# Kernel tuning notes

Measured on AMD Instinct MI355X. Metric: run time of the kernel, lower is better.

Reference implementation:

```python
import jax, jax.numpy as jnp
import numpy as np

EPS = 1e-5

def conv1x1(x, W, b):
    # x: (B,C,H,W), W: (O,C), b: (O,)
    return jnp.einsum('bchw,oc->bohw', x, W) + b[None, :, None, None]

def setup_inputs() -> dict:
    key = jax.random.key(0)
    ks = jax.random.split(key, 16)
    B, C_in, C1, D, K, H, Wd = 8, 512, 256, 128, 32, 96, 96
    s = lambda k, shape, fan: jax.random.normal(k, shape, jnp.float32) * (1.0 / np.sqrt(fan))
    return {
        'X': jax.random.normal(ks[0], (B, C_in, H, Wd), jnp.float32),
        'W_theta': s(ks[1], (C1, C_in), C_in), 'b_theta': jnp.zeros((C1,), jnp.float32),
        'W_phi': s(ks[2], (C1, C_in), C_in), 'b_phi': jnp.zeros((C1,), jnp.float32),
        'W_g': s(ks[3], (C1, C_in), C_in), 'b_g': jnp.zeros((C1,), jnp.float32),
        'W2': s(ks[4], (C_in, C1), C1), 'b2': jnp.zeros((C_in,), jnp.float32),
        'W3': s(ks[5], (D, C_in), C_in), 'b3': jnp.zeros((D,), jnp.float32),
        'codewords': jax.random.normal(ks[6], (K, D), jnp.float32),
        'scale': -jax.random.uniform(ks[7], (K,), jnp.float32),  # Deep-TEN init: U(-1,0)
        'W_fc': s(ks[8], (C_in, D), D), 'b_fc': jnp.zeros((C_in,), jnp.float32),
    }

def reference(X, W_theta, b_theta, W_phi, b_phi, W_g, b_g, W2, b2, W3, b3,
              codewords, scale, W_fc, b_fc):
    B, C_in, H, Wd = X.shape
    C1 = W_theta.shape[0]
    D, K = W3.shape[0], codewords.shape[0]
    N = H * Wd
    # --- non-local (channel-attention) block ---
    theta = conv1x1(X, W_theta, b_theta).reshape(B, C1, N)          # (B,C1,N)
    phi = conv1x1(X, W_phi, b_phi).reshape(B, C1, N)                # (B,C1,N)
    g = conv1x1(X, W_g, b_g).reshape(B, C1, N)                      # (B,C1,N)
    f = jax.nn.softmax(jnp.einsum('bcn,bdn->bcd', theta, phi), axis=-1)  # (B,C1,C1)
    y = jnp.einsum('bcd,bdn->bcn', f, g).reshape(B, C1, H, Wd)
    z = conv1x1(y, W2, b2) + X                                      # (B,C_in,H,W)
    # --- Deep-TEN encoding ---
    z_ = conv1x1(z, W3, b3)                                         # (B,D,H,W)
    x = z_.reshape(B, D, N).transpose(0, 2, 1)                      # (B,N,D)
    # squared L2 distances to codewords without (B,N,K,D) residuals
    dist = (jnp.sum(x * x, -1, keepdims=True)
            - 2.0 * jnp.einsum('bnd,kd->bnk', x, codewords)
            + jnp.sum(codewords * codewords, -1))                   # (B,N,K)
    A = jax.nn.softmax(scale * dist, axis=-1)                       # (B,N,K)
    # E_k = sum_i A_ik (x_i - c_k)
    E = jnp.einsum('bnk,bnd->bkd', A, x) - A.sum(1)[..., None] * codewords  # (B,K,D)
    # --- training-mode batch norm over K channels (no affine) ---
    mean = E.mean(axis=(0, 2), keepdims=True)
    var = E.var(axis=(0, 2), keepdims=True)
    e = jax.nn.relu((E - mean) * jax.lax.rsqrt(var + EPS))
    Es = e.sum(axis=1)                                              # (B,D)
    gamma = jax.nn.sigmoid(Es @ W_fc.T + b_fc)                      # (B,C_in)
    return z * gamma[:, :, None, None]
```

## Files before the change

kernel.cpp:

```cpp
#include <hip/hip_runtime.h>


typedef unsigned short u16;

#define Bb 8
#define Cc 512
#define C1 256
#define Dd 128
#define Kk 32
#define Nn 9216

typedef __attribute__((ext_vector_type(8))) short short8v;
typedef __attribute__((ext_vector_type(4))) short short4v;
typedef __attribute__((ext_vector_type(4))) float f32x4;

__device__ __forceinline__ float b2f(u16 u) {
  union { unsigned int i; float f; } v; v.i = ((unsigned int)u) << 16; return v.f;
}
__device__ __forceinline__ u16 f2b(float f) {
  union { float f; unsigned int i; } v; v.f = f;
  unsigned int x = v.i;
  return (u16)((x + 0x7fffu + ((x >> 16) & 1u)) >> 16);
}

__device__ __forceinline__ float4 load4(const float* p) { return *(const float4*)p; }
__device__ __forceinline__ float4 load4(const u16* p) {
  ushort4 q = *(const ushort4*)p;
  return make_float4(b2f(q.x), b2f(q.y), b2f(q.z), b2f(q.w));
}
__device__ __forceinline__ void store4(float* p, float a, float b, float c, float d) {
  *(float4*)p = make_float4(a, b, c, d);
}

__device__ __forceinline__ float waveSum(float v) {
  #pragma unroll
  for (int o = 32; o > 0; o >>= 1) v += __shfl_xor(v, o);
  return v;
}
__device__ __forceinline__ float waveMax(float v) {
  #pragma unroll
  for (int o = 32; o > 0; o >>= 1) v = fmaxf(v, __shfl_xor(v, o));
  return v;
}
__device__ __forceinline__ float blockSum256(float v) {
  __shared__ float sm[4];
  v = waveSum(v);
  if ((threadIdx.x & 63) == 0) sm[threadIdx.x >> 6] = v;
  __syncthreads();
  float r = sm[0] + sm[1] + sm[2] + sm[3];
  __syncthreads();
  return r;
}
__device__ __forceinline__ float blockMax256(float v) {
  __shared__ float sm[4];
  v = waveMax(v);
  if ((threadIdx.x & 63) == 0) sm[threadIdx.x >> 6] = v;
  __syncthreads();
  float r = fmaxf(fmaxf(sm[0], sm[1]), fmaxf(sm[2], sm[3]));
  __syncthreads();
  return r;
}

__device__ __forceinline__ f32x4 mfma_bf16_16x16x32(short8v a, short8v b, f32x4 c) {
  asm("v_mfma_f32_16x16x32_bf16 %0, %1, %2, %0" : "+v"(c) : "v"(a), "v"(b));
  return c;
}

__device__ __forceinline__ int fsw(int r) { return (r ^ (r >> 2) ^ (r >> 4)) & 3; }

__device__ __forceinline__ void cvt2(float x0, float x1, unsigned int& h, unsigned int& l) {
  asm("v_cvt_pk_bf16_f32 %0, %1, %2" : "=v"(h) : "v"(x0), "v"(x1));
  union { unsigned int u; float f; } fa, fb;
  fa.u = h << 16; fb.u = h & 0xffff0000u;
  float r0 = x0 - fa.f, r1 = x1 - fb.f;
  asm("v_cvt_pk_bf16_f32 %0, %1, %2" : "=v"(l) : "v"(r0), "v"(r1));
}

__device__ __forceinline__ void storeC4(float* p, float4 v) { *(float4*)p = v; }
__device__ __forceinline__ void storeC4(u16* p, float4 v) {
  ushort4 q; q.x = f2b(v.x); q.y = f2b(v.y); q.z = f2b(v.z); q.w = f2b(v.w);
  *(ushort4*)p = q;
}

template<typename TO, int NF, int OMODE>
__global__ __launch_bounds__(256, 2) void gemm_mfma(
    const float* __restrict__ A, const float* __restrict__ B, TO* __restrict__ C,
    int N, int K,
    long long sA, long long sB, long long sC,
    const float* __restrict__ biasRow, long long sBias,
    const float* __restrict__ scaleRow,
    int gnx, int gny)
{
  static_assert(NF == 8, "NF");
  constexpr int BN = 32 * NF;
  __shared__ __align__(16) u16 Asm_[2][128][40];
  __shared__ __align__(16) u16 Bsm_[2][BN][40];

  int id = blockIdx.x;
  {
    const int nwg = gridDim.x;
    if ((nwg & 7) == 0) id = (id & 7) * (nwg >> 3) + (id >> 3);
  }
  const int per = gnx * gny;
  const int b = id / per;
  const int rem = id - b * per;
  const int by = rem % gny;
  const int bx = rem / gny;
  A += b * sA; B += b * sB; C += b * sC;
  const int m0 = by * 128, n0 = bx * BN;

  const int t = threadIdx.x;
  const int w = t >> 6, lane = t & 63;
  const int wr = w >> 1, wc = w & 1;
  const int lr = lane & 15, lq = lane >> 4;

  const int sar = t >> 1, sak = (t & 1) * 16;
  const int kg = t >> 5, ng = t & 31;

  float ra[16];
  float rb[32];

  auto loadA = [&](int k0) {
    const float* p = A + (long long)(m0 + sar) * K + (k0 + sak);
    #pragma unroll
    for (int i = 0; i < 4; ++i) {
      float4 v = *(const float4*)(p + i * 4);
      ra[i*4+0] = v.x; ra[i*4+1] = v.y; ra[i*4+2] = v.z; ra[i*4+3] = v.w;
    }
  };
  auto loadB = [&](int k0) {
    const float* p = B + (long long)(k0 + kg * 4) * N + (n0 + ng * 8);
    #pragma unroll
    for (int i = 0; i < 4; ++i) {
      float4 v0 = *(const float4*)(p + (long long)i * N);
      float4 v1 = *(const float4*)(p + (long long)i * N + 4);
      rb[i*8+0]=v0.x; rb[i*8+1]=v0.y; rb[i*8+2]=v0.z; rb[i*8+3]=v0.w;
      rb[i*8+4]=v1.x; rb[i*8+5]=v1.y; rb[i*8+6]=v1.z; rb[i*8+7]=v1.w;
    }
  };

  auto stage = [&]() {
    {
      const int f = fsw(sar);
      #pragma unroll
      for (int h = 0; h < 2; ++h) {
        const int col = ((((sak >> 3) + h) ^ f) << 3);
        union { unsigned int u[4]; short8v v; } H, L;
        #pragma unroll
        for (int p = 0; p < 4; ++p) cvt2(ra[h*8+2*p], ra[h*8+2*p+1], H.u[p], L.u[p]);
        *(short8v*)&Asm_[0][sar][col] = H.v;
        *(short8v*)&Asm_[1][sar][col] = L.v;
      }
    }
    {
      #pragma unroll
      for (int j = 0; j < 8; ++j) {
        const int n = ng * 8 + j;
        const int col = (((kg >> 1) ^ fsw(n)) << 3) + (kg & 1) * 4;
        union { unsigned int u[2]; short4v v; } H, L;
        #pragma unroll
        for (int p = 0; p < 2; ++p)
          cvt2(rb[(2*p)*8 + j], rb[(2*p+1)*8 + j], H.u[p], L.u[p]);
        *(short4v*)&Bsm_[0][n][col] = H.v;
        *(short4v*)&Bsm_[1][n][col] = L.v;
      }
    }
  };

  f32x4 acc[4][NF];
  #pragma unroll
  for (int im = 0; im < 4; ++im)
    #pragma unroll
    for (int in = 0; in < NF; ++in)
      acc[im][in] = f32x4{0.f, 0.f, 0.f, 0.f};

  loadA(0); loadB(0);
  for (int k0 = 0; k0 < K; k0 += 32) {
    stage();
    if (k0 + 32 < K) { loadA(k0 + 32); loadB(k0 + 32); }
    __syncthreads();
    short8v af[2][4];
    #pragma unroll
    for (int im = 0; im < 4; ++im) {
      const int r = wr * 64 + im * 16 + lr;
      const int col = ((lq ^ fsw(r)) << 3);
      af[0][im] = *(const short8v*)&Asm_[0][r][col];
      af[1][im] = *(const short8v*)&Asm_[1][r][col];
    }
    #pragma unroll
    for (int in = 0; in < NF; ++in) {
      const int rB = wc * NF * 16 + in * 16 + lr;
      const int colB = ((lq ^ fsw(rB)) << 3);
      short8v bh = *(const short8v*)&Bsm_[0][rB][colB];
      short8v bl = *(const short8v*)&Bsm_[1][rB][colB];
      #pragma unroll
      for (int im = 0; im < 4; ++im) {
        acc[im][in] = mfma_bf16_16x16x32(af[0][im], bh, acc[im][in]);
        acc[im][in] = mfma_bf16_16x16x32(af[0][im], bl, acc[im][in]);
        acc[im][in] = mfma_bf16_16x16x32(af[1][im], bh, acc[im][in]);
      }
    }
    __syncthreads();
  }
  asm volatile("s_nop 7\n\ts_nop 7\n\ts_nop 7");

  if constexpr (OMODE == 1) {
    const float* bb = biasRow + (long long)b * sBias;
    #pragma unroll
    for (int im = 0; im < 4; ++im) {
      #pragma unroll
      for (int in = 0; in < NF; ++in) {
        const f32x4 a = acc[im][in];
        const int gc = n0 + wc * NF * 16 + in * 16 + lr;
        const int d0b = wr * 64 + im * 16 + lq * 4;
        float4 v = make_float4(a[0] + bb[d0b + 0], a[1] + bb[d0b + 1],
                               a[2] + bb[d0b + 2], a[3] + bb[d0b + 3]);
        storeC4(&C[(long long)gc * Dd + d0b], v);
      }
    }
  } else {
    #pragma unroll
    for (int im = 0; im < 4; ++im) {
      #pragma unroll
      for (int in = 0; in < NF; ++in) {
        const f32x4 a = acc[im][in];
        const int gc = n0 + wc * NF * 16 + in * 16 + lr;
        #pragma unroll
        for (int p = 0; p < 4; ++p) {
          const int gr = m0 + wr * 64 + im * 16 + lq * 4 + p;
          float v = a[p];
          if (biasRow) v += biasRow[b * sBias + gr];
          if (scaleRow) v *= scaleRow[b * sBias + gr];
          C[(long long)gr * N + gc] = v;
        }
      }
    }
  }
}

__device__ __constant__ int PIa[10] = {0,0,0,0,1,1,1,2,2,3};
__device__ __constant__ int PJa[10] = {0,1,2,3,1,2,3,2,3,3};

__global__ __launch_bounds__(256, 2) void gxxt_kernel(
    const float* __restrict__ X, float* __restrict__ part,
    int numKS, int kChunk)
{
  __shared__ __align__(16) u16 Asm_[2][128][40];
  __shared__ __align__(16) u16 Bsm_[2][128][40];

  int id = blockIdx.x;
  {
    const int nwg = gridDim.x;
    if ((nwg & 7) == 0) id = (id & 7) * (nwg >> 3) + (id >> 3);
  }
  const int pair = id % 10;
  const int rest = id / 10;
  const int ks = rest % numKS;
  const int b = rest / numKS;
  const int i0 = PIa[pair] * 128, j0 = PJa[pair] * 128;
  const bool same = (i0 == j0);
  const float* Xb = X + (long long)b * Cc * Nn;
  const int kBeg = ks * kChunk, kEnd = kBeg + kChunk;

  const int t = threadIdx.x;
  const int w = t >> 6, lane = t & 63;
  const int wr = w >> 1, wc = w & 1;
  const int lr = lane & 15, lq = lane >> 4;
  const int sar = t >> 1, sak = (t & 1) * 16;

  float ra[16], rb[16];

  auto loadA = [&](int k0) {
    const float* p = Xb + (long long)(i0 + sar) * Nn + (k0 + sak);
    #pragma unroll
    for (int i = 0; i < 4; ++i) {
      float4 v = *(const float4*)(p + i * 4);
      ra[i*4+0] = v.x; ra[i*4+1] = v.y; ra[i*4+2] = v.z; ra[i*4+3] = v.w;
    }
  };
  auto loadB = [&](int k0) {
    const float* p = Xb + (long long)(j0 + sar) * Nn + (k0 + sak);
    #pragma unroll
    for (int i = 0; i < 4; ++i) {
      float4 v = *(const float4*)(p + i * 4);
      rb[i*4+0] = v.x; rb[i*4+1] = v.y; rb[i*4+2] = v.z; rb[i*4+3] = v.w;
    }
  };
  auto stageRow = [&](const float* s16, u16 (*H)[40], u16 (*L)[40]) {
    const int f = fsw(sar);
    #pragma unroll
    for (int h = 0; h < 2; ++h) {
      const int col = ((((sak >> 3) + h) ^ f) << 3);
      union { unsigned int u[4]; short8v v; } Hv, Lv;
      #pragma unroll
      for (int p = 0; p < 4; ++p) cvt2(s16[h*8+2*p], s16[h*8+2*p+1], Hv.u[p], Lv.u[p]);
      *(short8v*)&H[sar][col] = Hv.v;
      *(short8v*)&L[sar][col] = Lv.v;
    }
  };

  const u16 (*BH)[40] = same ? Asm_[0] : Bsm_[0];
  const u16 (*BL)[40] = same ? Asm_[1] : Bsm_[1];

  f32x4 acc[4][4];
  #pragma unroll
  for (int im = 0; im < 4; ++im)
    #pragma unroll
    for (int in = 0; in < 4; ++in)
      acc[im][in] = f32x4{0.f, 0.f, 0.f, 0.f};

  loadA(kBeg);
  if (!same) loadB(kBeg);
  for (int k0 = kBeg; k0 < kEnd; k0 += 32) {
    stageRow(ra, Asm_[0], Asm_[1]);
    if (!same) stageRow(rb, Bsm_[0], Bsm_[1]);
    if (k0 + 32 < kEnd) { loadA(k0 + 32); if (!same) loadB(k0 + 32); }
    __syncthreads();
    short8v af[2][4];
    #pragma unroll
    for (int im = 0; im < 4; ++im) {
      const int r = wr * 64 + im * 16 + lr;
      const int col = ((lq ^ fsw(r)) << 3);
      af[0][im] = *(const short8v*)&Asm_[0][r][col];
      af[1][im] = *(const short8v*)&Asm_[1][r][col];
    }
    #pragma unroll
    for (int in = 0; in < 4; ++in) {
      const int rB = wc * 64 + in * 16 + lr;
      const int colB = ((lq ^ fsw(rB)) << 3);
      short8v bh = *(const short8v*)&BH[rB][colB];
      short8v bl = *(const short8v*)&BL[rB][colB];
      #pragma unroll
      for (int im = 0; im < 4; ++im) {
        acc[im][in] = mfma_bf16_16x16x32(af[0][im], bh, acc[im][in]);
        acc[im][in] = mfma_bf16_16x16x32(af[0][im], bl, acc[im][in]);
        acc[im][in] = mfma_bf16_16x16x32(af[1][im], bh, acc[im][in]);
      }
    }
    __syncthreads();
  }
  asm volatile("s_nop 7\n\ts_nop 7\n\ts_nop 7");

  float* Cp = part + ((long long)(ks * Bb + b) * 10 + pair) * 16384;
  #pragma unroll
  for (int im = 0; im < 4; ++im) {
    #pragma unroll
    for (int in = 0; in < 4; ++in) {
      const f32x4 a = acc[im][in];
      const int gc = wc * 64 + in * 16 + lr;
      #pragma unroll
      for (int p = 0; p < 4; ++p) {
        const int gr = wr * 64 + im * 16 + lq * 4 + p;
        Cp[gr * 128 + gc] = a[p];
      }
    }
  }
}

__global__ __launch_bounds__(256) void gred_kernel(const float* __restrict__ part,
    float* __restrict__ G, int numKS) {
  __shared__ float sm[64][129];
  const int pair = blockIdx.x % 10, b = blockIdx.x / 10;
  const int i0 = PIa[pair] * 128, j0 = PJa[pair] * 128;
  float* Gb = G + (long long)b * Cc * Cc;
  const long long ksStr = (long long)Bb * 10 * 16384;
  const float* p0 = part + ((long long)b * 10 + pair) * 16384;
  const int t = threadIdx.x;
  for (int half = 0; half < 2; ++half) {
    const int r0 = half * 64;
    __syncthreads();
    for (int rep = 0; rep < 32; ++rep) {
      int idx = r0 * 128 + rep * 256 + t;
      float s = 0.f;
      for (int ks = 0; ks < numKS; ++ks) s += p0[(long long)ks * ksStr + idx];
      int r = (idx >> 7) - r0, c = idx & 127;
      sm[r][c] = s;
      Gb[(long long)(i0 + r0 + r) * Cc + (j0 + c)] = s;
    }
    if (i0 != j0) {
      __syncthreads();
      for (int rep = 0; rep < 32; ++rep) {
        int o = rep * 256 + t;
        int rr = o >> 6, cc = o & 63;
        Gb[(long long)(j0 + rr) * Cc + (i0 + r0 + cc)] = sm[cc][rr];
      }
    }
  }
}

template<bool TRANSB>
__global__ __launch_bounds__(256) void gemm64(
    const float* __restrict__ A, const float* __restrict__ B, float* __restrict__ C,
    int M, int N, int K,
    long long sA, long long sB, long long sC,
    const float* __restrict__ biasRow, long long sBias)
{
  const int bz = blockIdx.z;
  A += (long long)bz * sA;
  B += (long long)bz * sB;
  C += (long long)bz * sC;
  const int m0 = blockIdx.y * 64, n0 = blockIdx.x * 64;
  __shared__ __align__(16) float As[16][64];
  __shared__ __align__(16) float Bs[16][64];
  const int t = threadIdx.x;
  const int lr = t >> 2, lk = (t & 3) << 2;
  const int tm = (t >> 4) << 2, tn = (t & 15) << 2;
  float acc[4][4] = {};
  for (int k0 = 0; k0 < K; k0 += 16) {
    {
      float4 a = load4(A + (long long)(m0 + lr) * K + (k0 + lk));
      As[lk + 0][lr] = a.x; As[lk + 1][lr] = a.y; As[lk + 2][lr] = a.z; As[lk + 3][lr] = a.w;
    }
    if (TRANSB) {
      float4 b = load4(B + (long long)(n0 + lr) * K + (k0 + lk));
      Bs[lk + 0][lr] = b.x; Bs[lk + 1][lr] = b.y; Bs[lk + 2][lr] = b.z; Bs[lk + 3][lr] = b.w;
    } else {
      const int kr = t >> 4, nc = (t & 15) << 2;
      float4 b = load4(B + (long long)(k0 + kr) * N + (n0 + nc));
      *(float4*)&Bs[kr][nc] = b;
    }
    __syncthreads();
    #pragma unroll
    for (int kk = 0; kk < 16; ++kk) {
      const float4 av = *(const float4*)&As[kk][tm];
      const float4 bv = *(const float4*)&Bs[kk][tn];
      acc[0][0] = fmaf(av.x, bv.x, acc[0][0]);
      acc[0][1] = fmaf(av.x, bv.y, acc[0][1]);
      acc[0][2] = fmaf(av.x, bv.z, acc[0][2]);
      acc[0][3] = fmaf(av.x, bv.w, acc[0][3]);
      acc[1][0] = fmaf(av.y, bv.x, acc[1][0]);
      acc[1][1] = fmaf(av.y, bv.y, acc[1][1]);
      acc[1][2] = fmaf(av.y, bv.z, acc[1][2]);
      acc[1][3] = fmaf(av.y, bv.w, acc[1][3]);
      acc[2][0] = fmaf(av.z, bv.x, acc[2][0]);
      acc[2][1] = fmaf(av.z, bv.y, acc[2][1]);
      acc[2][2] = fmaf(av.z, bv.z, acc[2][2]);
      acc[2][3] = fmaf(av.z, bv.w, acc[2][3]);
      acc[3][0] = fmaf(av.w, bv.x, acc[3][0]);
      acc[3][1] = fmaf(av.w, bv.y, acc[3][1]);
      acc[3][2] = fmaf(av.w, bv.z, acc[3][2]);
      acc[3][3] = fmaf(av.w, bv.w, acc[3][3]);
    }
    __syncthreads();
  }
  #pragma unroll
  for (int i = 0; i < 4; ++i) {
    const int m = m0 + tm + i;
    float bias = biasRow ? biasRow[bz * sBias + m] : 0.f;
    store4(C + (long long)m * N + (n0 + tn),
           acc[i][0] + bias, acc[i][1] + bias, acc[i][2] + bias, acc[i][3] + bias);
  }
}

__global__ __launch_bounds__(256) void rowsum_kernel(const float* __restrict__ X,
                                                     float* __restrict__ s, int N) {
  long long row = blockIdx.x;
  const float* p = X + row * N;
  float acc = 0.f;
  for (int i = threadIdx.x; i < N; i += 256) acc += p[i];
  acc = blockSum256(acc);
  if (threadIdx.x == 0) s[row] = acc;
}

__global__ __launch_bounds__(256) void gemv512_kernel(const float* __restrict__ W,
                                                      const float* __restrict__ s,
                                                      float* __restrict__ out) {
  int b = blockIdx.x;
  __shared__ float ssm[Cc];
  for (int i = threadIdx.x; i < Cc; i += 256) ssm[i] = s[b * Cc + i];
  __syncthreads();
  int i = threadIdx.x;
  const float* wr = W + i * Cc;
  float acc = 0.f;
  for (int k = 0; k < Cc; ++k) acc = fmaf(wr[k], ssm[k], acc);
  out[b * C1 + i] = acc;
}

__global__ __launch_bounds__(256) void softmax_kernel(float* __restrict__ L,
    const float* __restrict__ bth, const float* __restrict__ bph,
    const float* __restrict__ u, const float* __restrict__ v) {
  int row = blockIdx.x;
  int b = row >> 8, i = row & 255;
  int j = threadIdx.x;
  float bt = bth[i], bp = bph[j];
  long long idx = (long long)row * C1 + j;
  float val = L[idx] + bt * v[b * C1 + j] + u[b * C1 + i] * bp + (float)Nn * bt * bp;
  float mx = blockMax256(val);
  float p = expf(val - mx);
  float sm = blockSum256(p);
  L[idx] = p / sm;
}

__global__ __launch_bounds__(256) void w_kernel(const float* __restrict__ f,
                                                const float* __restrict__ bg,
                                                float* __restrict__ w) {
  int b = blockIdx.x;
  __shared__ float bgs[C1];
  bgs[threadIdx.x] = bg[threadIdx.x];
  __syncthreads();
  int i = threadIdx.x;
  const float* fr = f + ((long long)b * C1 + i) * C1;
  float acc = 0.f;
  for (int j = 0; j < C1; ++j) acc = fmaf(fr[j], bgs[j], acc);
  w[b * C1 + i] = acc;
}

__global__ __launch_bounds__(256) void q_kernel(const float* __restrict__ W2,
                                                const float* __restrict__ b2v,
                                                const float* __restrict__ w,
                                                float* __restrict__ q) {
  int gi = blockIdx.x * 256 + threadIdx.x;
  int b = gi >> 9, c = gi & 511;
  __shared__ float wsm[C1];
  wsm[threadIdx.x] = w[b * C1 + threadIdx.x];
  __syncthreads();
  const float* wr = W2 + c * C1;
  float acc = b2v[c];
  for (int i = 0; i < C1; ++i) acc = fmaf(wr[i], wsm[i], acc);
  q[gi] = acc;
}

__global__ __launch_bounds__(256) void adddiag_kernel(float* __restrict__ P) {
  int gi = blockIdx.x * 256 + threadIdx.x;
  int b = gi >> 9, c = gi & 511;
  P[((long long)b * Cc + c) * Cc + c] += 1.f;
}

__global__ __launch_bounds__(256) void zqbias_kernel(const float* __restrict__ W3,
    const float* __restrict__ b3, const float* __restrict__ q, float* __restrict__ zqb) {
  int gi = blockIdx.x * 256 + threadIdx.x;
  int b = gi >> 7, d = gi & 127;
  const float* wr = W3 + d * Cc;
  const float* qr = q + b * Cc;
  float acc = b3[d];
  for (int c = 0; c < Cc; ++c) acc = fmaf(wr[c], qr[c], acc);
  zqb[gi] = acc;
}

template<typename ZT>
__global__ __launch_bounds__(256) void enc_kernel(
    const ZT* __restrict__ zq,
    const float* __restrict__ cw,
    const float* __restrict__ sc,
    float* __restrict__ Eraw,
    float* __restrict__ Asum)
{
  __shared__ float csm[Kk][Dd + 1];
  __shared__ float cc[Kk], ssm[Kk];
  __shared__ float sA[Kk][256 + 1];
  __shared__ float zs[16][Dd + 4];
  const int tid = threadIdx.x;
  const int b = blockIdx.y;
  const int n0 = blockIdx.x * 256;

  #pragma unroll
  for (int r = 0; r < 16; ++r) {
    int idx = r * 256 + tid;
    csm[idx >> 7][idx & 127] = cw[idx];
  }
  if (tid < Kk) ssm[tid] = sc[tid];
  __syncthreads();
  if (tid < Kk) {
    float a = 0.f;
    for (int d = 0; d < Dd; ++d) { float cv = csm[tid][d]; a = fmaf(cv, cv, a); }
    cc[tid] = a;
  }
  __syncthreads();

  const ZT* zrow = zq + ((long long)b * Nn + n0 + tid) * Dd;
  float dots[Kk];
  #pragma unroll
  for (int k = 0; k < Kk; ++k) dots[k] = 0.f;
  float xx = 0.f;
  for (int d = 0; d < Dd; d += 4) {
    float4 xv = load4(zrow + d);
    xx = fmaf(xv.x, xv.x, xx); xx = fmaf(xv.y, xv.y, xx);
    xx = fmaf(xv.z, xv.z, xx); xx = fmaf(xv.w, xv.w, xx);
    #pragma unroll
    for (int k = 0; k < Kk; ++k) {
      float dk = dots[k];
      dk = fmaf(csm[k][d + 0], xv.x, dk);
      dk = fmaf(csm[k][d + 1], xv.y, dk);
      dk = fmaf(csm[k][d + 2], xv.z, dk);
      dk = fmaf(csm[k][d + 3], xv.w, dk);
      dots[k] = dk;
    }
  }
  float mx = -1e30f;
  #pragma unroll
  for (int k = 0; k < Kk; ++k) {
    float l = ssm[k] * (xx - 2.f * dots[k] + cc[k]);
    dots[k] = l;
    mx = fmaxf(mx, l);
  }
  float sum = 0.f;
  #pragma unroll
  for (int k = 0; k < Kk; ++k) { float p = expf(dots[k] - mx); dots[k] = p; sum += p; }
  float inv = 1.f / sum;
  #pragma unroll
  for (int k = 0; k < Kk; ++k) sA[k][tid] = dots[k] * inv;
  __syncthreads();
  if (tid < Kk) {
    float s = 0.f;
    for (int p = 0; p < 256; ++p) s += sA[tid][p];
    atomicAdd(&Asum[b * Kk + tid], s);
  }

  float acc[16];
  #pragma unroll
  for (int j = 0; j < 16; ++j) acc[j] = 0.f;
  const int k = tid & 31, d0 = (tid >> 5) * 16;
  const int spx = tid >> 4, sd = (tid & 15) * 8;
  for (int it = 0; it < 16; ++it) {
    __syncthreads();
    {
      const ZT* src = zq + ((long long)b * Nn + n0 + it * 16 + spx) * Dd + sd;
      float4 a4 = load4(src);
      float4 b4 = load4(src + 4);
      *(float4*)&zs[spx][sd] = a4;
      *(float4*)&zs[spx][sd + 4] = b4;
    }
    __syncthreads();
    #pragma unroll
    for (int p = 0; p < 16; ++p) {
      float a = sA[k][it * 16 + p];
      #pragma unroll
      for (int j = 0; j < 16; ++j) acc[j] = fmaf(a, zs[p][d0 + j], acc[j]);
    }
  }
  float* Ep = Eraw + ((long long)b * Kk + k) * Dd + d0;
  #pragma unroll
  for (int j = 0; j < 16; ++j) atomicAdd(Ep + j, acc[j]);
}

__global__ __launch_bounds__(256) void bn_kernel(const float* __restrict__ Eraw,
    const float* __restrict__ Asum, const float* __restrict__ cw, float* __restrict__ Es) {
  int k = blockIdx.x, tid = threadIdx.x;
  float vals[4], s = 0.f, s2 = 0.f;
  #pragma unroll
  for (int r = 0; r < 4; ++r) {
    int i = r * 256 + tid;
    int b = i >> 7, d = i & 127;
    float e = Eraw[((long long)b * Kk + k) * Dd + d] - Asum[b * Kk + k] * cw[k * Dd + d];
    vals[r] = e; s += e; s2 = fmaf(e, e, s2);
  }
  s = blockSum256(s);
  s2 = blockSum256(s2);
  float mean = s * (1.f / 1024.f);
  float var = fmaxf(s2 * (1.f / 1024.f) - mean * mean, 0.f);
  float rs = rsqrtf(var + 1e-5f);
  #pragma unroll
  for (int r = 0; r < 4; ++r) {
    int i = r * 256 + tid;
    int b = i >> 7, d = i & 127;
    float e = (vals[r] - mean) * rs;
    if (e > 0.f) atomicAdd(&Es[b * Dd + d], e);
  }
}

__global__ __launch_bounds__(256) void gamma_kernel(const float* __restrict__ Es,
    const float* __restrict__ Wfc, const float* __restrict__ bfc, float* __restrict__ gam) {
  int gi = blockIdx.x * 256 + threadIdx.x;
  int b = gi >> 9, c = gi & 511;
  __shared__ float esm[Dd];
  if (threadIdx.x < Dd) esm[threadIdx.x] = Es[b * Dd + threadIdx.x];
  __syncthreads();
  const float* wr = Wfc + c * Dd;
  float acc = bfc[c];
  for (int d = 0; d < Dd; ++d) acc = fmaf(wr[d], esm[d], acc);
  gam[gi] = 1.f / (1.f + expf(-acc));
}

extern "C" void kernel_launch(void* const* d_in, const int* in_sizes, int n_in,
                              void* d_out, int out_size, void* d_ws, size_t ws_size,
                              hipStream_t stream) {
  const float* X   = (const float*)d_in[0];
  const float* Wth = (const float*)d_in[1];
  const float* bth = (const float*)d_in[2];
  const float* Wph = (const float*)d_in[3];
  const float* bph = (const float*)d_in[4];
  const float* Wg  = (const float*)d_in[5];
  const float* bg  = (const float*)d_in[6];
  const float* W2  = (const float*)d_in[7];
  const float* b2v = (const float*)d_in[8];
  const float* W3  = (const float*)d_in[9];
  const float* b3v = (const float*)d_in[10];
  const float* CW  = (const float*)d_in[11];
  const float* SC  = (const float*)d_in[12];
  const float* Wfc = (const float*)d_in[13];
  const float* bfc = (const float*)d_in[14];
  float* out = (float*)d_out;
  float* wsf = (float*)d_ws;

  const long long szL   = (long long)Bb * C1 * C1;
  const long long szRA  = (long long)Bb * Cc * Cc;
  const long long szRB  = (long long)Bb * C1 * Cc;
  long long off = 0;
  float* s_   = wsf + off; off += Bb * Cc;
  float* u_   = wsf + off; off += Bb * C1;
  float* v_   = wsf + off; off += Bb * C1;
  float* w_   = wsf + off; off += Bb * C1;
  float* q_   = wsf + off; off += Bb * Cc;
  float* Eraw_= wsf + off; off += (long long)Bb * Kk * Dd;
  float* Es_  = wsf + off; off += Bb * Dd;
  float* Asum_= wsf + off; off += Bb * Kk;
  float* gam_ = wsf + off; off += Bb * Cc;
  float* L_   = wsf + off; off += szL;
  float* regA = wsf + off; off += szRA;
  float* regB = wsf + off; off += szRB;
  const long long baseFloats = off;
  float* tail = wsf + off;
  const long long ZQ_F  = (long long)Bb * Dd * Nn;
  const long long tailFloats = (long long)(ws_size / 4) - baseFloats;
  const bool big = tailFloats >= ZQ_F;
  const int numKS = big ? 6 : 2;
  float* part = tail;
  float* zqf  = tail;
  u16*   zqh  = (u16*)tail;
  float* R_   = L_;
  float* zqb_ = u_;

  const long long strX = (long long)Cc * Nn;
  const long long sG = (long long)Cc * Cc;
  const long long sU = (long long)C1 * Cc;
  const long long sL = (long long)C1 * C1;
  const long long sR = (long long)Dd * Cc;

  rowsum_kernel<<<Bb * Cc, 256, 0, stream>>>(X, s_, Nn);
  gxxt_kernel<<<dim3(10 * numKS * Bb), 256, 0, stream>>>(X, part, numKS, Nn / numKS);
  gred_kernel<<<dim3(10 * Bb), 256, 0, stream>>>(part, regA, numKS);
  gemm_mfma<float, 8, 0><<<dim3(32), 256, 0, stream>>>(
      Wth, regA, regB, Cc, Cc, 0, sG, sU, nullptr, 0, nullptr, 2, 2);
  gemv512_kernel<<<Bb, 256, 0, stream>>>(Wth, s_, u_);
  gemv512_kernel<<<Bb, 256, 0, stream>>>(Wph, s_, v_);
  gemm64<true><<<dim3(4, 4, Bb), 256, 0, stream>>>(
      regB, Wph, L_, C1, C1, Cc, sU, 0, sL, nullptr, 0);
  softmax_kernel<<<Bb * C1, 256, 0, stream>>>(L_, bth, bph, u_, v_);
  w_kernel<<<Bb, 256, 0, stream>>>(L_, bg, w_);
  gemm_mfma<float, 8, 0><<<dim3(32), 256, 0, stream>>>(
      L_, Wg, regB, Cc, C1, sL, 0, sU, nullptr, 0, nullptr, 2, 2);
  q_kernel<<<16, 256, 0, stream>>>(W2, b2v, w_, q_);
  gemm_mfma<float, 8, 0><<<dim3(64), 256, 0, stream>>>(
      W2, regB, regA, Cc, C1, 0, sU, sG, nullptr, 0, nullptr, 2, 4);
  adddiag_kernel<<<16, 256, 0, stream>>>(regA);
  gemm_mfma<float, 8, 0><<<dim3(16), 256, 0, stream>>>(
      W3, regA, R_, Cc, Cc, 0, sG, sR, nullptr, 0, nullptr, 2, 1);
  zqbias_kernel<<<4, 256, 0, stream>>>(W3, b3v, q_, zqb_);
  hipMemsetAsync(Eraw_, 0, (size_t)(Bb * Kk * Dd + Bb * Dd + Bb * Kk) * 4, stream);
  if (big) {
    gemm_mfma<float, 8, 1><<<dim3(288), 256, 0, stream>>>(
        R_, X, zqf, Nn, Cc, sR, strX, (long long)Dd * Nn, zqb_, Dd, nullptr, 36, 1);
    enc_kernel<float><<<dim3(36, Bb), 256, 0, stream>>>(zqf, CW, SC, Eraw_, Asum_);
  } else {
    gemm_mfma<u16, 8, 1><<<dim3(288), 256, 0, stream>>>(
        R_, X, zqh, Nn, Cc, sR, strX, (long long)Dd * Nn, zqb_, Dd, nullptr, 36, 1);
    enc_kernel<u16><<<dim3(36, Bb), 256, 0, stream>>>(zqh, CW, SC, Eraw_, Asum_);
  }
  bn_kernel<<<Kk, 256, 0, stream>>>(Eraw_, Asum_, CW, Es_);
  gamma_kernel<<<16, 256, 0, stream>>>(Es_, Wfc, bfc, gam_);
  gemm_mfma<float, 8, 0><<<dim3(1152), 256, 0, stream>>>(
      regA, X, out, Nn, Cc, sG, strX, strX, q_, Cc, gam_, 36, 4);
  (void)in_sizes; (void)n_in; (void)out_size;
}
```

Before: 1.096 ms.

## Fuse small kernels, fold gamma into P, and spread encoding atomics over slots

Merges the two gemv launches into one and folds the w reduction into the softmax kernel. The +I diagonal moves into the W2 GEMM epilogue, and gamma is pre-applied to P and q so the final GEMM epilogue no longer scales each element. The encoding accumulators are split into 8 slot copies that bn_kernel reduces, which cuts atomic contention in enc_kernel. This trades a few launches and the per-element scale load for an extra pass over P (scaleP) and a larger zeroing memset.

```diff
diff --git a/kernel.cpp b/kernel.cpp
--- a/kernel.cpp
+++ b/kernel.cpp
@@ -82,13 +82,12 @@
   *(ushort4*)p = q;
 }
 
-template<typename TO, int NF, int OMODE>
+template<typename TO, int NF, int OMODE, bool ADDI>
 __global__ __launch_bounds__(256, 2) void gemm_mfma(
     const float* __restrict__ A, const float* __restrict__ B, TO* __restrict__ C,
     int N, int K,
     long long sA, long long sB, long long sC,
     const float* __restrict__ biasRow, long long sBias,
-    const float* __restrict__ scaleRow,
     int gnx, int gny)
 {
   static_assert(NF == 8, "NF");
@@ -230,7 +229,7 @@
           const int gr = m0 + wr * 64 + im * 16 + lq * 4 + p;
           float v = a[p];
           if (biasRow) v += biasRow[b * sBias + gr];
-          if (scaleRow) v *= scaleRow[b * sBias + gr];
+          if (ADDI && gr == gc) v += 1.f;
           C[(long long)gr * N + gc] = v;
         }
       }
@@ -462,10 +461,12 @@
   if (threadIdx.x == 0) s[row] = acc;
 }
 
-__global__ __launch_bounds__(256) void gemv512_kernel(const float* __restrict__ W,
-                                                      const float* __restrict__ s,
-                                                      float* __restrict__ out) {
-  int b = blockIdx.x;
+__global__ __launch_bounds__(256) void gemv2_kernel(const float* __restrict__ Wth,
+    const float* __restrict__ Wph, const float* __restrict__ s,
+    float* __restrict__ u, float* __restrict__ v) {
+  int b = blockIdx.x & 7, sel = blockIdx.x >> 3;
+  const float* W = sel ? Wph : Wth;
+  float* out = sel ? v : u;
   __shared__ float ssm[Cc];
   for (int i = threadIdx.x; i < Cc; i += 256) ssm[i] = s[b * Cc + i];
   __syncthreads();
@@ -478,31 +479,23 @@
 
 __global__ __launch_bounds__(256) void softmax_kernel(float* __restrict__ L,
     const float* __restrict__ bth, const float* __restrict__ bph,
-    const float* __restrict__ u, const float* __restrict__ v) {
+    const float* __restrict__ u, const float* __restrict__ v,
+    const float* __restrict__ bg, float* __restrict__ w) {
+  __shared__ float bgs[C1];
   int row = blockIdx.x;
   int b = row >> 8, i = row & 255;
   int j = threadIdx.x;
+  bgs[j] = bg[j];
   float bt = bth[i], bp = bph[j];
   long long idx = (long long)row * C1 + j;
   float val = L[idx] + bt * v[b * C1 + j] + u[b * C1 + i] * bp + (float)Nn * bt * bp;
   float mx = blockMax256(val);
   float p = expf(val - mx);
   float sm = blockSum256(p);
-  L[idx] = p / sm;
-}
-
-__global__ __launch_bounds__(256) void w_kernel(const float* __restrict__ f,
-                                                const float* __restrict__ bg,
-                                                float* __restrict__ w) {
-  int b = blockIdx.x;
-  __shared__ float bgs[C1];
-  bgs[threadIdx.x] = bg[threadIdx.x];
-  __syncthreads();
-  int i = threadIdx.x;
-  const float* fr = f + ((long long)b * C1 + i) * C1;
-  float acc = 0.f;
-  for (int j = 0; j < C1; ++j) acc = fmaf(fr[j], bgs[j], acc);
-  w[b * C1 + i] = acc;
+  float f = p / sm;
+  L[idx] = f;
+  float ws = blockSum256(f * bgs[j]);
+  if (j == 0) w[row] = ws;
 }
 
 __global__ __launch_bounds__(256) void q_kernel(const float* __restrict__ W2,
@@ -518,12 +511,6 @@
   float acc = b2v[c];
   for (int i = 0; i < C1; ++i) acc = fmaf(wr[i], wsm[i], acc);
   q[gi] = acc;
-}
-
-__global__ __launch_bounds__(256) void adddiag_kernel(float* __restrict__ P) {
-  int gi = blockIdx.x * 256 + threadIdx.x;
-  int b = gi >> 9, c = gi & 511;
-  P[((long long)b * Cc + c) * Cc + c] += 1.f;
 }
 
 __global__ __launch_bounds__(256) void zqbias_kernel(const float* __restrict__ W3,
@@ -542,8 +529,8 @@
     const ZT* __restrict__ zq,
     const float* __restrict__ cw,
     const float* __restrict__ sc,
-    float* __restrict__ Eraw,
-    float* __restrict__ Asum)
+    float* __restrict__ Eraw8,
+    float* __restrict__ Asum8)
 {
   __shared__ float csm[Kk][Dd + 1];
   __shared__ float cc[Kk], ssm[Kk];
@@ -551,6 +538,7 @@
   __shared__ float zs[16][Dd + 4];
   const int tid = threadIdx.x;
   const int b = blockIdx.y;
+  const int slot = blockIdx.x & 7;
   const int n0 = blockIdx.x * 256;
 
   #pragma unroll
@@ -603,7 +591,7 @@
   if (tid < Kk) {
     float s = 0.f;
     for (int p = 0; p < 256; ++p) s += sA[tid][p];
-    atomicAdd(&Asum[b * Kk + tid], s);
+    atomicAdd(&Asum8[((long long)slot * Bb + b) * Kk + tid], s);
   }
 
   float acc[16];
@@ -628,20 +616,30 @@
       for (int j = 0; j < 16; ++j) acc[j] = fmaf(a, zs[p][d0 + j], acc[j]);
     }
   }
-  float* Ep = Eraw + ((long long)b * Kk + k) * Dd + d0;
+  float* Ep = Eraw8 + (((long long)slot * Bb + b) * Kk + k) * Dd + d0;
   #pragma unroll
   for (int j = 0; j < 16; ++j) atomicAdd(Ep + j, acc[j]);
 }
 
-__global__ __launch_bounds__(256) void bn_kernel(const float* __restrict__ Eraw,
-    const float* __restrict__ Asum, const float* __restrict__ cw, float* __restrict__ Es) {
+__global__ __launch_bounds__(256) void bn_kernel(const float* __restrict__ Eraw8,
+    const float* __restrict__ Asum8, const float* __restrict__ cw, float* __restrict__ Es) {
+  __shared__ float sas[8];
   int k = blockIdx.x, tid = threadIdx.x;
+  if (tid < 8) {
+    float a = 0.f;
+    for (int sl = 0; sl < 8; ++sl) a += Asum8[((long long)sl * Bb + tid) * Kk + k];
+    sas[tid] = a;
+  }
+  __syncthreads();
   float vals[4], s = 0.f, s2 = 0.f;
   #pragma unroll
   for (int r = 0; r < 4; ++r) {
     int i = r * 256 + tid;
     int b = i >> 7, d = i & 127;
-    float e = Eraw[((long long)b * Kk + k) * Dd + d] - Asum[b * Kk + k] * cw[k * Dd + d];
+    float e = 0.f;
+    for (int sl = 0; sl < 8; ++sl)
+      e += Eraw8[(((long long)sl * Bb + b) * Kk + k) * Dd + d];
+    e -= sas[b] * cw[k * Dd + d];
     vals[r] = e; s += e; s2 = fmaf(e, e, s2);
   }
   s = blockSum256(s);
@@ -659,7 +657,8 @@
 }
 
 __global__ __launch_bounds__(256) void gamma_kernel(const float* __restrict__ Es,
-    const float* __restrict__ Wfc, const float* __restrict__ bfc, float* __restrict__ gam) {
+    const float* __restrict__ Wfc, const float* __restrict__ bfc,
+    float* __restrict__ gam, float* __restrict__ q) {
   int gi = blockIdx.x * 256 + threadIdx.x;
   int b = gi >> 9, c = gi & 511;
   __shared__ float esm[Dd];
@@ -668,7 +667,18 @@
   const float* wr = Wfc + c * Dd;
   float acc = bfc[c];
   for (int d = 0; d < Dd; ++d) acc = fmaf(wr[d], esm[d], acc);
-  gam[gi] = 1.f / (1.f + expf(-acc));
+  float g = 1.f / (1.f + expf(-acc));
+  gam[gi] = g;
+  q[gi] *= g;
+}
+
+__global__ __launch_bounds__(256) void scaleP_kernel(float* __restrict__ P,
+    const float* __restrict__ gam) {
+  long long f = ((long long)blockIdx.x * 256 + threadIdx.x) * 4;
+  int b = (int)(f >> 18), c = (int)((f >> 9) & 511);
+  float g = gam[b * Cc + c];
+  float4 v = *(const float4*)(P + f);
+  store4(P + f, v.x * g, v.y * g, v.z * g, v.w * g);
 }
 
 extern "C" void kernel_launch(void* const* d_in, const int* in_sizes, int n_in,
@@ -719,6 +729,9 @@
   u16*   zqh  = (u16*)tail;
   float* R_   = L_;
   float* zqb_ = u_;
+  float* E8_  = regB;
+  float* A8_  = regB + 262144;
+  (void)Eraw_; (void)Asum_;
 
   const long long strX = (long long)Cc * Nn;
   const long long sG = (long long)Cc * Cc;
@@ -729,36 +742,35 @@
   rowsum_kernel<<<Bb * Cc, 256, 0, stream>>>(X, s_, Nn);
   gxxt_kernel<<<dim3(10 * numKS * Bb), 256, 0, stream>>>(X, part, numKS, Nn / numKS);
   gred_kernel<<<dim3(10 * Bb), 256, 0, stream>>>(part, regA, numKS);
-  gemm_mfma<float, 8, 0><<<dim3(32), 256, 0, stream>>>(
-      Wth, regA, regB, Cc, Cc, 0, sG, sU, nullptr, 0, nullptr, 2, 2);
-  gemv512_kernel<<<Bb, 256, 0, stream>>>(Wth, s_, u_);
-  gemv512_kernel<<<Bb, 256, 0, stream>>>(Wph, s_, v_);
+  gemm_mfma<float, 8, 0, false><<<dim3(32), 256, 0, stream>>>(
+      Wth, regA, regB, Cc, Cc, 0, sG, sU, nullptr, 0, 2, 2);
+  gemv2_kernel<<<16, 256, 0, stream>>>(Wth, Wph, s_, u_, v_);
   gemm64<true><<<dim3(4, 4, Bb), 256, 0, stream>>>(
       regB, Wph, L_, C1, C1, Cc, sU, 0, sL, nullptr, 0);
-  softmax_kernel<<<Bb * C1, 256, 0, stream>>>(L_, bth, bph, u_, v_);
-  w_kernel<<<Bb, 256, 0, stream>>>(L_, bg, w_);
-  gemm_mfma<float, 8, 0><<<dim3(32), 256, 0, stream>>>(
-      L_, Wg, regB, Cc, C1, sL, 0, sU, nullptr, 0, nullptr, 2, 2);
+  softmax_kernel<<<Bb * C1, 256, 0, stream>>>(L_, bth, bph, u_, v_, bg, w_);
+  gemm_mfma<float, 8, 0, false><<<dim3(32), 256, 0, stream>>>(
+      L_, Wg, regB, Cc, C1, sL, 0, sU, nullptr, 0, 2, 2);
   q_kernel<<<16, 256, 0, stream>>>(W2, b2v, w_, q_);
-  gemm_mfma<float, 8, 0><<<dim3(64), 256, 0, stream>>>(
-      W2, regB, regA, Cc, C1, 0, sU, sG, nullptr, 0, nullptr, 2, 4);
-  adddiag_kernel<<<16, 256, 0, stream>>>(regA);
-  gemm_mfma<float, 8, 0><<<dim3(16), 256, 0, stream>>>(
-      W3, regA, R_, Cc, Cc, 0, sG, sR, nullptr, 0, nullptr, 2, 1);
+  gemm_mfma<float, 8, 0, true><<<dim3(64), 256, 0, stream>>>(
+      W2, regB, regA, Cc, C1, 0, sU, sG, nullptr, 0, 2, 4);
+  hipMemsetAsync(regB, 0, (size_t)(262144 + 2048) * 4, stream);
+  hipMemsetAsync(Es_, 0, (size_t)(Bb * Dd) * 4, stream);
+  gemm_mfma<float, 8, 0, false><<<dim3(16), 256, 0, stream>>>(
+      W3, regA, R_, Cc, Cc, 0, sG, sR, nullptr, 0, 2, 1);
   zqbias_kernel<<<4, 256, 0, stream>>>(W3, b3v, q_, zqb_);
-  hipMemsetAsync(Eraw_, 0, (size_t)(Bb * Kk * Dd + Bb * Dd + Bb * Kk) * 4, stream);
   if (big) {
-    gemm_mfma<float, 8, 1><<<dim3(288), 256, 0, stream>>>(
-        R_, X, zqf, Nn, Cc, sR, strX, (long long)Dd * Nn, zqb_, Dd, nullptr, 36, 1);
-    enc_kernel<float><<<dim3(36, Bb), 256, 0, stream>>>(zqf, CW, SC, Eraw_, Asum_);
+    gemm_mfma<float, 8, 1, false><<<dim3(288), 256, 0, stream>>>(
+        R_, X, zqf, Nn, Cc, sR, strX, (long long)Dd * Nn, zqb_, Dd, 36, 1);
+    enc_kernel<float><<<dim3(36, Bb), 256, 0, stream>>>(zqf, CW, SC, E8_, A8_);
   } else {
-    gemm_mfma<u16, 8, 1><<<dim3(288), 256, 0, stream>>>(
-        R_, X, zqh, Nn, Cc, sR, strX, (long long)Dd * Nn, zqb_, Dd, nullptr, 36, 1);
-    enc_kernel<u16><<<dim3(36, Bb), 256, 0, stream>>>(zqh, CW, SC, Eraw_, Asum_);
-  }
-  bn_kernel<<<Kk, 256, 0, stream>>>(Eraw_, Asum_, CW, Es_);
-  gamma_kernel<<<16, 256, 0, stream>>>(Es_, Wfc, bfc, gam_);
-  gemm_mfma<float, 8, 0><<<dim3(1152), 256, 0, stream>>>(
-      regA, X, out, Nn, Cc, sG, strX, strX, q_, Cc, gam_, 36, 4);
+    gemm_mfma<u16, 8, 1, false><<<dim3(288), 256, 0, stream>>>(
+        R_, X, zqh, Nn, Cc, sR, strX, (long long)Dd * Nn, zqb_, Dd, 36, 1);
+    enc_kernel<u16><<<dim3(36, Bb), 256, 0, stream>>>(zqh, CW, SC, E8_, A8_);
+  }
+  bn_kernel<<<Kk, 256, 0, stream>>>(E8_, A8_, CW, Es_);
+  gamma_kernel<<<16, 256, 0, stream>>>(Es_, Wfc, bfc, gam_, q_);
+  scaleP_kernel<<<2048, 256, 0, stream>>>(regA, gam_);
+  gemm_mfma<float, 8, 0, false><<<dim3(1152), 256, 0, stream>>>(
+      regA, X, out, Nn, Cc, sG, strX, strX, q_, Cc, 36, 4);
   (void)in_sizes; (void)n_in; (void)out_size;
 }
```

New measurement: 1.039 ms. 5.1% less time.
